# Performance work log

Measured on AMD Instinct MI355X. Metric: run time of the kernel, lower is better.

Reference implementation:

```python
import jax, jax.numpy as jnp
import numpy as np
import math

B, H, N, K, D = 4, 8, 4096, 32, 8  # batch, heads, points, neighbors, head depth (k_out/H)


def setup_inputs() -> dict:
    key = jax.random.key(0)
    ks = jax.random.split(key, 6)
    return {
        "q": jax.random.normal(ks[0], (B, H, N, 1, D), dtype=jnp.float32),
        "k_mat": jax.random.normal(ks[1], (B, H, N, D, K), dtype=jnp.float32),
        "v": jax.random.normal(ks[2], (B, H, N, K, D), dtype=jnp.float32),
        "re_xyz": jax.random.normal(ks[3], (B, N, K, 3), dtype=jnp.float32),
        "w1": jax.random.normal(ks[4], (3, H), dtype=jnp.float32) * 0.5,  # linear1: 3 -> num_heads
        "b1": jnp.zeros((H,), dtype=jnp.float32),
        "w2": jax.random.normal(ks[5], (3, H * D), dtype=jnp.float32) * 0.5,  # linear2: 3 -> k_out
        "b2": jnp.zeros((H * D,), dtype=jnp.float32),
    }


def reference(q, k_mat, v, re_xyz, w1, b1, w2, b2):
    # pe_ii positional bias on attention scores: [B,N,K,3] -> [B,N,K,H] -> [B,H,N,1,K]
    q_xyz = re_xyz @ w1 + b1
    q_xyz = jnp.transpose(q_xyz, (0, 3, 1, 2))[:, :, :, None, :]
    # energy: [B,H,N,1,D] @ [B,H,N,D,K] -> [B,H,N,1,K]
    energy = jnp.matmul(q, k_mat) + q_xyz
    scale = math.sqrt(q.shape[-1])
    attention = jax.nn.softmax(energy / scale, axis=-1)
    # value positional term: [B,N,K,H*D] raw-reshaped to [B,H,N,K,D] (matches torch .view)
    v_xyz = (re_xyz @ w2 + b2).reshape(v.shape[0], H, v.shape[2], v.shape[3], D)
    v = v + v_xyz
    # [B,H,N,1,K] @ [B,H,N,K,D] -> [B,H,N,1,D] -> [B,N,H,D]
    x = jnp.matmul(attention, v)[:, :, :, 0, :].transpose(0, 2, 1, 3)
    return x
```

## Files before the change

kernel.cpp:

```cpp
#include <hip/hip_runtime.h>
#include <math.h>


#define T_PER_BLOCK 16

__global__ __launch_bounds__(512, 1) void pe_attn_kernel(
    const float* __restrict__ q,
    const float* __restrict__ k_mat,
    const float* __restrict__ v,
    const float* __restrict__ re_xyz,
    const float* __restrict__ w1,
    const float* __restrict__ b1,
    const float* __restrict__ w2,
    const float* __restrict__ b2,
    float* __restrict__ out)
{
    __shared__ __align__(16) float lds_k[T_PER_BLOCK * 256];

    const int tid  = threadIdx.x;
    const int wave = tid >> 6;
    const int lane = tid & 63;
    const int t0   = blockIdx.x * T_PER_BLOCK;

    #pragma unroll
    for (int j = 0; j < 2; ++j) {
        const int seg = wave * 2 + j;
        __builtin_amdgcn_global_load_lds(
            (const __attribute__((address_space(1))) void*)
                (k_mat + (size_t)t0 * 256 + seg * 256 + lane * 4),
            (__attribute__((address_space(3))) void*)(lds_k + seg * 256),
            16, 0, 0);
    }

    const int it  = tid >> 5;
    const int k   = tid & 31;
    const int t   = t0 + it;
    const int b   = t >> 15;
    const int rem = t & 32767;
    const int h   = rem >> 12;
    const int n   = rem & 4095;

    const float* vbase = v + (size_t)t * 256 + k * 8;
    const float4 v0 = ((const float4*)vbase)[0];
    const float4 v1 = ((const float4*)vbase)[1];

    const size_t rxb = ((size_t)((b << 12) + n) * 32 + k) * 3;
    const float rx0 = re_xyz[rxb], rx1 = re_xyz[rxb + 1], rx2 = re_xyz[rxb + 2];

    const int n2 = rem >> 3;
    const int k2 = ((rem & 7) << 2) + (k >> 3);
    const size_t rxb2 = ((size_t)((b << 12) + n2) * 32 + k2) * 3;
    const float s0 = re_xyz[rxb2], s1 = re_xyz[rxb2 + 1], s2 = re_xyz[rxb2 + 2];

    const float4 qa = ((const float4*)(q + (size_t)t * 8))[0];
    const float4 qb = ((const float4*)(q + (size_t)t * 8))[1];

    const float wq0 = w1[h], wq1 = w1[8 + h], wq2 = w1[16 + h], bq = b1[h];
    const int c0 = (k & 7) << 3;
    const float4 wr0a = ((const float4*)(w2 + c0))[0];
    const float4 wr0b = ((const float4*)(w2 + c0))[1];
    const float4 wr1a = ((const float4*)(w2 + 64 + c0))[0];
    const float4 wr1b = ((const float4*)(w2 + 64 + c0))[1];
    const float4 wr2a = ((const float4*)(w2 + 128 + c0))[0];
    const float4 wr2b = ((const float4*)(w2 + 128 + c0))[1];
    const float4 bba  = ((const float4*)(b2 + c0))[0];
    const float4 bbb  = ((const float4*)(b2 + c0))[1];

    __syncthreads();

    const float* kt = lds_k + it * 256;
    float e = qa.x * kt[k]
            + qa.y * kt[32  + k]
            + qa.z * kt[64  + k]
            + qa.w * kt[96  + k]
            + qb.x * kt[128 + k]
            + qb.y * kt[160 + k]
            + qb.z * kt[192 + k]
            + qb.w * kt[224 + k];
    e += rx0 * wq0 + rx1 * wq1 + rx2 * wq2 + bq;
    e *= 0.35355339059327373f;
    const float p = __expf(e);

    float s = p;
    #pragma unroll
    for (int off = 16; off; off >>= 1) s += __shfl_xor(s, off);

    float pd[8];
    pd[0] = p * (v0.x + s0 * wr0a.x + s1 * wr1a.x + s2 * wr2a.x + bba.x);
    pd[1] = p * (v0.y + s0 * wr0a.y + s1 * wr1a.y + s2 * wr2a.y + bba.y);
    pd[2] = p * (v0.z + s0 * wr0a.z + s1 * wr1a.z + s2 * wr2a.z + bba.z);
    pd[3] = p * (v0.w + s0 * wr0a.w + s1 * wr1a.w + s2 * wr2a.w + bba.w);
    pd[4] = p * (v1.x + s0 * wr0b.x + s1 * wr1b.x + s2 * wr2b.x + bbb.x);
    pd[5] = p * (v1.y + s0 * wr0b.y + s1 * wr1b.y + s2 * wr2b.y + bbb.y);
    pd[6] = p * (v1.z + s0 * wr0b.z + s1 * wr1b.z + s2 * wr2b.z + bbb.z);
    pd[7] = p * (v1.w + s0 * wr0b.w + s1 * wr1b.w + s2 * wr2b.w + bbb.w);

    {
        const bool hb = (k & 16) != 0;
        #pragma unroll
        for (int j = 0; j < 4; ++j) {
            float send = hb ? pd[j] : pd[j + 4];
            float recv = __shfl_xor(send, 16);
            pd[j] = (hb ? pd[j + 4] : pd[j]) + recv;
        }
    }
    {
        const bool hb = (k & 8) != 0;
        #pragma unroll
        for (int j = 0; j < 2; ++j) {
            float send = hb ? pd[j] : pd[j + 2];
            float recv = __shfl_xor(send, 8);
            pd[j] = (hb ? pd[j + 2] : pd[j]) + recv;
        }
    }
    {
        const bool hb = (k & 4) != 0;
        float send = hb ? pd[0] : pd[1];
        float recv = __shfl_xor(send, 4);
        pd[0] = (hb ? pd[1] : pd[0]) + recv;
    }
    pd[0] += __shfl_xor(pd[0], 2);
    pd[0] += __shfl_xor(pd[0], 1);

    if ((k & 3) == 0) {
        const int d = (k >> 2) & 7;
        out[((size_t)((b << 12) + n) * 8 + h) * 8 + d] =
            pd[0] * __builtin_amdgcn_rcpf(s);
    }
}

extern "C" void kernel_launch(void* const* d_in, const int* in_sizes, int n_in,
                              void* d_out, int out_size, void* d_ws, size_t ws_size,
                              hipStream_t stream) {
    const float* q      = (const float*)d_in[0];
    const float* k_mat  = (const float*)d_in[1];
    const float* v      = (const float*)d_in[2];
    const float* re_xyz = (const float*)d_in[3];
    const float* w1     = (const float*)d_in[4];
    const float* b1     = (const float*)d_in[5];
    const float* w2     = (const float*)d_in[6];
    const float* b2     = (const float*)d_in[7];
    float* out = (float*)d_out;

    dim3 grid(131072 / T_PER_BLOCK), block(512);
    hipLaunchKernelGGL(pe_attn_kernel, grid, block, 0, stream,
                       q, k_mat, v, re_xyz, w1, b1, w2, b2, out);
}
```

Baseline: 289.3 us.

## Loop each 32-lane group over eight rows with register double-buffered prefetch

Replaces one-row-per-group blocks, which staged k_mat through LDS, with persistent-style groups of 32 lanes. Each group processes eight consecutive (b,h,n) rows and prefetches the next row's k, q, v and re_xyz into registers while computing the current one. The LDS staging and the block barrier are removed, and k_mat is read directly with strided scalar loads. The per-block weight loads are amortised across rows. Risks are higher register pressure, fewer and smaller blocks (2048 x 256), and less coalesced k_mat access.

```diff
diff --git a/kernel.cpp b/kernel.cpp
--- a/kernel.cpp
+++ b/kernel.cpp
@@ -2,9 +2,39 @@
 #include <math.h>
 
 
-#define T_PER_BLOCK 16
+#define GROUPS_PER_BLOCK 8
+#define TRIP_PER_GROUP   8
+#define NBLOCKS          2048
 
-__global__ __launch_bounds__(512, 1) void pe_attn_kernel(
+struct Tri {
+    float k0,k1,k2,k3,k4,k5,k6,k7;
+    float4 qa, qb;
+    float r0,r1,r2;
+    float s0,s1,s2;
+    float4 v0, v1;
+};
+
+__device__ __forceinline__ Tri load_tri(
+    const float* __restrict__ q, const float* __restrict__ k_mat,
+    const float* __restrict__ v, const float* __restrict__ re_xyz,
+    int t, int b, int n, int k, const float* __restrict__ rxc_row, int i)
+{
+    Tri x;
+    const float* kb = k_mat + (size_t)t * 256 + k;
+    x.k0 = kb[0];   x.k1 = kb[32];  x.k2 = kb[64];  x.k3 = kb[96];
+    x.k4 = kb[128]; x.k5 = kb[160]; x.k6 = kb[192]; x.k7 = kb[224];
+    const float4* qp = (const float4*)(q + (size_t)t * 8);
+    x.qa = qp[0]; x.qb = qp[1];
+    const float* rb = re_xyz + ((size_t)((b << 12) + n) * 32 + k) * 3;
+    x.r0 = rb[0]; x.r1 = rb[1]; x.r2 = rb[2];
+    const float* rc = rxc_row + 12 * i;
+    x.s0 = rc[0]; x.s1 = rc[1]; x.s2 = rc[2];
+    const float4* vb = (const float4*)(v + (size_t)t * 256 + (k << 3));
+    x.v0 = vb[0]; x.v1 = vb[1];
+    return x;
+}
+
+__global__ __launch_bounds__(256, 4) void pe_attn_kernel(
     const float* __restrict__ q,
     const float* __restrict__ k_mat,
     const float* __restrict__ v,
@@ -15,45 +45,15 @@
     const float* __restrict__ b2,
     float* __restrict__ out)
 {
-    __shared__ __align__(16) float lds_k[T_PER_BLOCK * 256];
-
-    const int tid  = threadIdx.x;
-    const int wave = tid >> 6;
-    const int lane = tid & 63;
-    const int t0   = blockIdx.x * T_PER_BLOCK;
-
-    #pragma unroll
-    for (int j = 0; j < 2; ++j) {
-        const int seg = wave * 2 + j;
-        __builtin_amdgcn_global_load_lds(
-            (const __attribute__((address_space(1))) void*)
-                (k_mat + (size_t)t0 * 256 + seg * 256 + lane * 4),
-            (__attribute__((address_space(3))) void*)(lds_k + seg * 256),
-            16, 0, 0);
-    }
-
-    const int it  = tid >> 5;
+    const int tid = threadIdx.x;
     const int k   = tid & 31;
-    const int t   = t0 + it;
-    const int b   = t >> 15;
-    const int rem = t & 32767;
-    const int h   = rem >> 12;
-    const int n   = rem & 4095;
-
-    const float* vbase = v + (size_t)t * 256 + k * 8;
-    const float4 v0 = ((const float4*)vbase)[0];
-    const float4 v1 = ((const float4*)vbase)[1];
-
-    const size_t rxb = ((size_t)((b << 12) + n) * 32 + k) * 3;
-    const float rx0 = re_xyz[rxb], rx1 = re_xyz[rxb + 1], rx2 = re_xyz[rxb + 2];
-
-    const int n2 = rem >> 3;
-    const int k2 = ((rem & 7) << 2) + (k >> 3);
-    const size_t rxb2 = ((size_t)((b << 12) + n2) * 32 + k2) * 3;
-    const float s0 = re_xyz[rxb2], s1 = re_xyz[rxb2 + 1], s2 = re_xyz[rxb2 + 2];
-
-    const float4 qa = ((const float4*)(q + (size_t)t * 8))[0];
-    const float4 qb = ((const float4*)(q + (size_t)t * 8))[1];
+    const int g   = blockIdx.x * GROUPS_PER_BLOCK + (tid >> 5);
+    const int t0  = g * TRIP_PER_GROUP;
+    const int b   = t0 >> 15;
+    const int rem0= t0 & 32767;
+    const int h   = rem0 >> 12;
+    const int n0  = rem0 & 4095;
+    const int n2  = rem0 >> 3;
 
     const float wq0 = w1[h], wq1 = w1[8 + h], wq2 = w1[16 + h], bq = b1[h];
     const int c0 = (k & 7) << 3;
@@ -65,67 +65,73 @@
     const float4 wr2b = ((const float4*)(w2 + 128 + c0))[1];
     const float4 bba  = ((const float4*)(b2 + c0))[0];
     const float4 bbb  = ((const float4*)(b2 + c0))[1];
+    const float* rxc_row = re_xyz + ((size_t)((b << 12) + n2) * 32 + (k >> 3)) * 3;
 
-    __syncthreads();
+    Tri cur = load_tri(q, k_mat, v, re_xyz, t0, b, n0, k, rxc_row, 0);
 
-    const float* kt = lds_k + it * 256;
-    float e = qa.x * kt[k]
-            + qa.y * kt[32  + k]
-            + qa.z * kt[64  + k]
-            + qa.w * kt[96  + k]
-            + qb.x * kt[128 + k]
-            + qb.y * kt[160 + k]
-            + qb.z * kt[192 + k]
-            + qb.w * kt[224 + k];
-    e += rx0 * wq0 + rx1 * wq1 + rx2 * wq2 + bq;
-    e *= 0.35355339059327373f;
-    const float p = __expf(e);
+    #pragma unroll
+    for (int i = 0; i < TRIP_PER_GROUP; ++i) {
+        Tri nxt;
+        if (i < TRIP_PER_GROUP - 1)
+            nxt = load_tri(q, k_mat, v, re_xyz, t0 + i + 1, b, n0 + i + 1, k,
+                           rxc_row, i + 1);
 
-    float s = p;
-    #pragma unroll
-    for (int off = 16; off; off >>= 1) s += __shfl_xor(s, off);
+        float e = cur.qa.x * cur.k0 + cur.qa.y * cur.k1
+                + cur.qa.z * cur.k2 + cur.qa.w * cur.k3
+                + cur.qb.x * cur.k4 + cur.qb.y * cur.k5
+                + cur.qb.z * cur.k6 + cur.qb.w * cur.k7;
+        e += cur.r0 * wq0 + cur.r1 * wq1 + cur.r2 * wq2 + bq;
+        e *= 0.35355339059327373f;
+        const float p = __expf(e);
 
-    float pd[8];
-    pd[0] = p * (v0.x + s0 * wr0a.x + s1 * wr1a.x + s2 * wr2a.x + bba.x);
-    pd[1] = p * (v0.y + s0 * wr0a.y + s1 * wr1a.y + s2 * wr2a.y + bba.y);
-    pd[2] = p * (v0.z + s0 * wr0a.z + s1 * wr1a.z + s2 * wr2a.z + bba.z);
-    pd[3] = p * (v0.w + s0 * wr0a.w + s1 * wr1a.w + s2 * wr2a.w + bba.w);
-    pd[4] = p * (v1.x + s0 * wr0b.x + s1 * wr1b.x + s2 * wr2b.x + bbb.x);
-    pd[5] = p * (v1.y + s0 * wr0b.y + s1 * wr1b.y + s2 * wr2b.y + bbb.y);
-    pd[6] = p * (v1.z + s0 * wr0b.z + s1 * wr1b.z + s2 * wr2b.z + bbb.z);
-    pd[7] = p * (v1.w + s0 * wr0b.w + s1 * wr1b.w + s2 * wr2b.w + bbb.w);
+        float s = p;
+        #pragma unroll
+        for (int off = 16; off; off >>= 1) s += __shfl_xor(s, off);
 
-    {
-        const bool hb = (k & 16) != 0;
-        #pragma unroll
-        for (int j = 0; j < 4; ++j) {
-            float send = hb ? pd[j] : pd[j + 4];
-            float recv = __shfl_xor(send, 16);
-            pd[j] = (hb ? pd[j + 4] : pd[j]) + recv;
+        float pd[8];
+        pd[0] = p * (cur.v0.x + cur.s0*wr0a.x + cur.s1*wr1a.x + cur.s2*wr2a.x + bba.x);
+        pd[1] = p * (cur.v0.y + cur.s0*wr0a.y + cur.s1*wr1a.y + cur.s2*wr2a.y + bba.y);
+        pd[2] = p * (cur.v0.z + cur.s0*wr0a.z + cur.s1*wr1a.z + cur.s2*wr2a.z + bba.z);
+        pd[3] = p * (cur.v0.w + cur.s0*wr0a.w + cur.s1*wr1a.w + cur.s2*wr2a.w + bba.w);
+        pd[4] = p * (cur.v1.x + cur.s0*wr0b.x + cur.s1*wr1b.x + cur.s2*wr2b.x + bbb.x);
+        pd[5] = p * (cur.v1.y + cur.s0*wr0b.y + cur.s1*wr1b.y + cur.s2*wr2b.y + bbb.y);
+        pd[6] = p * (cur.v1.z + cur.s0*wr0b.z + cur.s1*wr1b.z + cur.s2*wr2b.z + bbb.z);
+        pd[7] = p * (cur.v1.w + cur.s0*wr0b.w + cur.s1*wr1b.w + cur.s2*wr2b.w + bbb.w);
+
+        {
+            const bool hb = (k & 16) != 0;
+            #pragma unroll
+            for (int j = 0; j < 4; ++j) {
+                float send = hb ? pd[j] : pd[j + 4];
+                float recv = __shfl_xor(send, 16);
+                pd[j] = (hb ? pd[j + 4] : pd[j]) + recv;
+            }
         }
-    }
-    {
-        const bool hb = (k & 8) != 0;
-        #pragma unroll
-        for (int j = 0; j < 2; ++j) {
-            float send = hb ? pd[j] : pd[j + 2];
-            float recv = __shfl_xor(send, 8);
-            pd[j] = (hb ? pd[j + 2] : pd[j]) + recv;
+        {
+            const bool hb = (k & 8) != 0;
+            #pragma unroll
+            for (int j = 0; j < 2; ++j) {
+                float send = hb ? pd[j] : pd[j + 2];
+                float recv = __shfl_xor(send, 8);
+                pd[j] = (hb ? pd[j + 2] : pd[j]) + recv;
+            }
         }
-    }
-    {
-        const bool hb = (k & 4) != 0;
-        float send = hb ? pd[0] : pd[1];
-        float recv = __shfl_xor(send, 4);
-        pd[0] = (hb ? pd[1] : pd[0]) + recv;
-    }
-    pd[0] += __shfl_xor(pd[0], 2);
-    pd[0] += __shfl_xor(pd[0], 1);
+        {
+            const bool hb = (k & 4) != 0;
+            float send = hb ? pd[0] : pd[1];
+            float recv = __shfl_xor(send, 4);
+            pd[0] = (hb ? pd[1] : pd[0]) + recv;
+        }
+        pd[0] += __shfl_xor(pd[0], 2);
+        pd[0] += __shfl_xor(pd[0], 1);
 
-    if ((k & 3) == 0) {
-        const int d = (k >> 2) & 7;
-        out[((size_t)((b << 12) + n) * 8 + h) * 8 + d] =
-            pd[0] * __builtin_amdgcn_rcpf(s);
+        if ((k & 3) == 0) {
+            const int d = (k >> 2) & 7;
+            out[((size_t)((b << 12) + (n0 + i)) * 8 + h) * 8 + d] =
+                pd[0] * __builtin_amdgcn_rcpf(s);
+        }
+
+        cur = nxt;
     }
 }
 
@@ -142,7 +148,7 @@
     const float* b2     = (const float*)d_in[7];
     float* out = (float*)d_out;
 
-    dim3 grid(131072 / T_PER_BLOCK), block(512);
+    dim3 grid(NBLOCKS), block(256);
     hipLaunchKernelGGL(pe_attn_kernel, grid, block, 0, stream,
                        q, k_mat, v, re_xyz, w1, b1, w2, b2, out);
 }
```

New measurement: 291.3 us. No clear change (+0.7%).
